# Kernel optimization log

Measured on AMD Instinct MI355X. Metric: run time of the kernel, lower is better.

## Reference

```python
import jax, jax.numpy as jnp
import numpy as np

HIDDEN = 768
B = 32
GRID_X, GRID_Y = 84, 30          # 84*30 = 2520 input patches
SEQ = GRID_X * GRID_Y            # 2520
OUT_LEN = 280                    # 2520 // 280 = 9 -> k = 3


def setup_inputs() -> dict:
    key = jax.random.key(0)
    k1, k2 = jax.random.split(key)
    hidden_states = jax.random.normal(k1, (B, SEQ, HIDDEN), dtype=jnp.float32)
    # (x, y) grid coordinates for each patch, identical across batch
    x = jnp.arange(SEQ, dtype=jnp.int32) % GRID_X
    y = jnp.arange(SEQ, dtype=jnp.int32) // GRID_X
    pos = jnp.stack([x, y], axis=-1)                     # [SEQ, 2]
    pixel_position_ids = jnp.broadcast_to(pos, (B, SEQ, 2))
    padding_positions = jax.random.bernoulli(k2, 0.05, (B, SEQ))  # bool mask
    return {
        "hidden_states": hidden_states,
        "pixel_position_ids": pixel_position_ids,
        "padding_positions": padding_positions,
        "output_length": OUT_LEN,
    }


def reference(hidden_states, pixel_position_ids, padding_positions, output_length):
    root_hidden_size = hidden_states.shape[-1] ** 0.5
    # zero out padded patches
    hs = jnp.where(padding_positions[..., None], 0.0, hidden_states)
    seq_len = hs.shape[1]
    if seq_len != output_length:
        k = int((seq_len // output_length) ** 0.5)
        k_squared = k * k
        clamped = jnp.maximum(pixel_position_ids, 0)            # [B, S, 2]
        max_x = jnp.max(clamped[..., 0], axis=-1, keepdims=True) + 1  # [B, 1]
        kidx = clamped // k
        seg = kidx[..., 0] + (max_x // k) * kidx[..., 1]        # [B, S] bucket ids
        hs32 = hs.astype(jnp.float32)
        # segment-sum per batch == one_hot(seg).T @ hs, without the dense one-hot
        pooled = jax.vmap(
            lambda h, i: jax.ops.segment_sum(h, i, num_segments=output_length)
        )(hs32, seg) / k_squared                                 # [B, L, H]
        counts = jax.vmap(
            lambda i: jax.ops.segment_sum(jnp.ones_like(i), i, num_segments=output_length)
        )(seg)                                                   # [B, L]
        mask = counts > 0  # bucket received at least one patch (one-hot col nonzero)
        hs = pooled.astype(hidden_states.dtype)
        padding_positions = mask
    hs = hs * root_hidden_size
    return hs, padding_positions
```

## Files before the change

### kernel.cpp

```cpp
#include <hip/hip_runtime.h>
#include <math.h>


#define NB    32
#define SEQL  2520
#define HID   768
#define OUTL  280
#define CAP   16
#define GX    84
#define KP    3
#define MXK   (GX / KP)

typedef float f32x4 __attribute__((ext_vector_type(4)));

__global__ void __launch_bounds__(256)
k_verify(const int* __restrict__ pos, const int* __restrict__ padding,
         int* __restrict__ flags, int* __restrict__ ents,
         float* __restrict__ out_mask) {
    __shared__ int r_ok[256];
    __shared__ int r_mx[256];
    __shared__ int s_cnt[OUTL];
    __shared__ int s_ent[OUTL * CAP];
    const int b = blockIdx.x;
    const int t = threadIdx.x;
    const int* p = pos + (size_t)b * SEQL * 2;

    int ok = 1, m = 0;
    for (int s = t; s < SEQL; s += 256) {
        int x = p[2 * s], y = p[2 * s + 1];
        ok &= (x == s % GX) & (y == s / GX);
        int cx = x < 0 ? 0 : x;
        if (cx > m) m = cx;
    }
    r_ok[t] = ok; r_mx[t] = m;
    __syncthreads();
    for (int off = 128; off > 0; off >>= 1) {
        if (t < off) {
            r_ok[t] &= r_ok[t + off];
            int o = r_mx[t + off]; if (o > r_mx[t]) r_mx[t] = o;
        }
        __syncthreads();
    }
    if (r_ok[0]) {
        if (t == 0) flags[b] = 1;
        return;
    }

    const int mxk = (r_mx[0] + 1) / KP;
    for (int i = t; i < OUTL; i += 256) s_cnt[i] = 0;
    for (int i = t; i < OUTL * CAP; i += 256) s_ent[i] = 1;
    __syncthreads();
    const int* pd = padding + (size_t)b * SEQL;
    for (int s = t; s < SEQL; s += 256) {
        int x = p[2 * s];     if (x < 0) x = 0;
        int y = p[2 * s + 1]; if (y < 0) y = 0;
        int seg = x / KP + mxk * (y / KP);
        if (seg >= 0 && seg < OUTL) {
            int slot = atomicAdd(&s_cnt[seg], 1);
            if (slot < CAP)
                s_ent[seg * CAP + slot] = (s << 1) | (pd[s] != 0 ? 1 : 0);
        }
    }
    __syncthreads();
    int* eg = ents + (size_t)b * OUTL * CAP;
    for (int i = t; i < OUTL * CAP; i += 256) eg[i] = s_ent[i];
    for (int i = t; i < OUTL; i += 256)
        out_mask[b * OUTL + i] = (s_cnt[i] > 0) ? 1.0f : 0.0f;
    if (t == 0) flags[b] = 0;
}

__global__ void __launch_bounds__(192)
k_pool(const float* __restrict__ hs, const int* __restrict__ padding,
       const int* __restrict__ flags, const int* __restrict__ ents,
       float* __restrict__ out, float* __restrict__ out_mask, float scale) {
    __shared__ int se[9];
    const int l = blockIdx.x;
    const int b = blockIdx.y;
    const int bl = b * OUTL + l;

    if (flags[b]) {
        if ((int)threadIdx.x < 9) {
            int dy = threadIdx.x / 3, dx = threadIdx.x - 3 * dy;
            int s = (KP * (l / MXK) + dy) * GX + KP * (l % MXK) + dx;
            se[threadIdx.x] = (s << 1) | (padding[b * SEQL + s] != 0 ? 1 : 0);
        }
        if (threadIdx.x == 0) out_mask[bl] = 1.0f;
    } else if (threadIdx.x == 0) {
        int e[9];
        const int* eg = ents + (size_t)bl * CAP;
        #pragma unroll
        for (int i = 0; i < 9; ++i) e[i] = eg[i];
        #pragma unroll
        for (int i = 1; i < 9; ++i) {
            int v = e[i], j = i - 1;
            while (j >= 0 && e[j] > v) { e[j + 1] = e[j]; --j; }
            e[j + 1] = v;
        }
        #pragma unroll
        for (int i = 0; i < 9; ++i) se[i] = e[i];
    }
    __syncthreads();

    f32x4 acc = (f32x4)(0.f);
    const f32x4* base = (const f32x4*)(hs + (size_t)b * SEQL * HID);
    #pragma unroll
    for (int i = 0; i < 9; ++i) {
        int e = se[i];
        if (!(e & 1)) {
            f32x4 v = __builtin_nontemporal_load(
                base + (size_t)(e >> 1) * (HID / 4) + threadIdx.x);
            acc += v;
        }
    }
    acc *= scale;
    __builtin_nontemporal_store(acc,
        (f32x4*)(out + (size_t)bl * HID) + threadIdx.x);
}

extern "C" void kernel_launch(void* const* d_in, const int* in_sizes, int n_in,
                              void* d_out, int out_size, void* d_ws, size_t ws_size,
                              hipStream_t stream) {
    const float* hs      = (const float*)d_in[0];
    const int*   pos     = (const int*)d_in[1];
    const int*   padding = (const int*)d_in[2];

    int* flags = (int*)d_ws;
    int* ents  = (int*)((char*)d_ws + 128);

    float* out      = (float*)d_out;
    float* out_mask = out + (size_t)NB * OUTL * HID;
    const float scale = sqrtf((float)HID) / 9.0f;

    k_verify<<<NB, 256, 0, stream>>>(pos, padding, flags, ents, out_mask);
    dim3 grid(OUTL, NB);
    k_pool<<<grid, 192, 0, stream>>>(hs, padding, flags, ents, out, out_mask, scale);
}
```

Measured before the change: 51.33 us.

## Pool four output buckets per block and vectorize position verification loads

Each pooling block now handles four adjacent output buckets along x. It loads the 3x12 padding tile once and issues all 36 row loads in an unrolled loop, so each block has more memory requests in flight and a quarter as many blocks launch. The verify kernel reads positions as int4, covering two patches per load. The trade-off is higher register use from four accumulators and reduced grid parallelism (70x32 blocks).

```diff
diff --git a/kernel.cpp b/kernel.cpp
--- a/kernel.cpp
+++ b/kernel.cpp
@@ -10,6 +10,8 @@
 #define GX    84
 #define KP    3
 #define MXK   (GX / KP)
+#define LPB   4
+#define GPR   (MXK / LPB)
 
 typedef float f32x4 __attribute__((ext_vector_type(4)));
 
@@ -24,13 +26,16 @@
     const int b = blockIdx.x;
     const int t = threadIdx.x;
     const int* p = pos + (size_t)b * SEQL * 2;
+    const int4* p4 = (const int4*)p;
 
     int ok = 1, m = 0;
-    for (int s = t; s < SEQL; s += 256) {
-        int x = p[2 * s], y = p[2 * s + 1];
-        ok &= (x == s % GX) & (y == s / GX);
-        int cx = x < 0 ? 0 : x;
-        if (cx > m) m = cx;
+    for (int i = t; i < SEQL / 2; i += 256) {
+        int4 v = p4[i];
+        int s0 = 2 * i, s1 = 2 * i + 1;
+        ok &= (v.x == s0 % GX) & (v.y == s0 / GX)
+            & (v.z == s1 % GX) & (v.w == s1 / GX);
+        int cx = v.x < 0 ? 0 : v.x; if (cx > m) m = cx;
+        cx = v.z < 0 ? 0 : v.z;     if (cx > m) m = cx;
     }
     r_ok[t] = ok; r_mx[t] = m;
     __syncthreads();
@@ -73,21 +78,26 @@
 k_pool(const float* __restrict__ hs, const int* __restrict__ padding,
        const int* __restrict__ flags, const int* __restrict__ ents,
        float* __restrict__ out, float* __restrict__ out_mask, float scale) {
-    __shared__ int se[9];
-    const int l = blockIdx.x;
+    __shared__ int spad[3 * 3 * LPB];
+    __shared__ int se[LPB][9];
+    const int g = blockIdx.x;
     const int b = blockIdx.y;
-    const int bl = b * OUTL + l;
+    const int t = threadIdx.x;
+    const int yk = g / GPR;
+    const int x0 = (g % GPR) * KP * LPB;
+    const int l0 = yk * MXK + (g % GPR) * LPB;
+    const int fast = flags[b];
 
-    if (flags[b]) {
-        if ((int)threadIdx.x < 9) {
-            int dy = threadIdx.x / 3, dx = threadIdx.x - 3 * dy;
-            int s = (KP * (l / MXK) + dy) * GX + KP * (l % MXK) + dx;
-            se[threadIdx.x] = (s << 1) | (padding[b * SEQL + s] != 0 ? 1 : 0);
+    if (fast) {
+        if (t < 3 * 3 * LPB) {
+            int dy = t / (3 * LPB), j = t % (3 * LPB);
+            int s = (KP * yk + dy) * GX + x0 + j;
+            spad[t] = (padding[b * SEQL + s] != 0);
         }
-        if (threadIdx.x == 0) out_mask[bl] = 1.0f;
-    } else if (threadIdx.x == 0) {
+        if (t < LPB) out_mask[b * OUTL + l0 + t] = 1.0f;
+    } else if (t < LPB) {
         int e[9];
-        const int* eg = ents + (size_t)bl * CAP;
+        const int* eg = ents + ((size_t)b * OUTL + l0 + t) * CAP;
         #pragma unroll
         for (int i = 0; i < 9; ++i) e[i] = eg[i];
         #pragma unroll
@@ -97,24 +107,49 @@
             e[j + 1] = v;
         }
         #pragma unroll
-        for (int i = 0; i < 9; ++i) se[i] = e[i];
+        for (int i = 0; i < 9; ++i) se[t][i] = e[i];
     }
     __syncthreads();
 
-    f32x4 acc = (f32x4)(0.f);
+    f32x4 acc[LPB];
+    #pragma unroll
+    for (int q = 0; q < LPB; ++q) acc[q] = (f32x4)(0.f);
     const f32x4* base = (const f32x4*)(hs + (size_t)b * SEQL * HID);
-    #pragma unroll
-    for (int i = 0; i < 9; ++i) {
-        int e = se[i];
-        if (!(e & 1)) {
-            f32x4 v = __builtin_nontemporal_load(
-                base + (size_t)(e >> 1) * (HID / 4) + threadIdx.x);
-            acc += v;
+
+    if (fast) {
+        #pragma unroll
+        for (int dy = 0; dy < 3; ++dy) {
+            const int row_s = (KP * yk + dy) * GX + x0;
+            #pragma unroll
+            for (int j = 0; j < 3 * LPB; ++j) {
+                if (!spad[dy * 3 * LPB + j]) {
+                    f32x4 v = __builtin_nontemporal_load(
+                        base + (size_t)(row_s + j) * (HID / 4) + t);
+                    acc[j / KP] += v;
+                }
+            }
+        }
+    } else {
+        #pragma unroll
+        for (int q = 0; q < LPB; ++q) {
+            #pragma unroll
+            for (int i = 0; i < 9; ++i) {
+                int e = se[q][i];
+                if (!(e & 1)) {
+                    f32x4 v = __builtin_nontemporal_load(
+                        base + (size_t)(e >> 1) * (HID / 4) + t);
+                    acc[q] += v;
+                }
+            }
         }
     }
-    acc *= scale;
-    __builtin_nontemporal_store(acc,
-        (f32x4*)(out + (size_t)bl * HID) + threadIdx.x);
+
+    f32x4* og = (f32x4*)(out + (size_t)(b * OUTL + l0) * HID) + t;
+    #pragma unroll
+    for (int q = 0; q < LPB; ++q) {
+        acc[q] *= scale;
+        __builtin_nontemporal_store(acc[q], og + (size_t)q * (HID / 4));
+    }
 }
 
 extern "C" void kernel_launch(void* const* d_in, const int* in_sizes, int n_in,
@@ -132,6 +167,6 @@
     const float scale = sqrtf((float)HID) / 9.0f;
 
     k_verify<<<NB, 256, 0, stream>>>(pos, padding, flags, ents, out_mask);
-    dim3 grid(OUTL, NB);
+    dim3 grid(OUTL / LPB / (MXK / LPB) * GPR, NB);
     k_pool<<<grid, 192, 0, stream>>>(hs, padding, flags, ents, out, out_mask, scale);
 }
```

Measured after the change: 63.89 us. 24.5% more time.
